# Kernel optimization log

Measured on AMD Instinct MI355X. Metric: run time of the kernel, lower is better.

## Reference

```python
import jax, jax.numpy as jnp
import numpy as np
import math

B, S, D, L, FF = 16, 2048, 512, 4, 2048
VOCAB, ATTR_VOCAB, MAXPOS = 33, 608, 2048
EPS = 1e-5


def layernorm(x, w, b):
    mu = jnp.mean(x, axis=-1, keepdims=True)
    var = jnp.mean(jnp.square(x - mu), axis=-1, keepdims=True)
    return (x - mu) * jax.lax.rsqrt(var + EPS) * w + b


def setup_inputs() -> dict:
    key = jax.random.key(0)
    ks = jax.random.split(key, 16)
    std = 0.02
    return {
        "input_ids": jax.random.randint(ks[0], (B, S), 0, VOCAB),
        "combined_indices": jax.random.randint(ks[1], (B,), 0, ATTR_VOCAB),
        "attention_mask": jnp.ones((B, S), dtype=jnp.float32),
        "tok_emb": jax.random.normal(ks[2], (VOCAB, D), jnp.float32) * std,
        "pos_emb": jax.random.normal(ks[3], (MAXPOS, D), jnp.float32) * std,
        "attr_emb": jax.random.normal(ks[4], (ATTR_VOCAB, D), jnp.float32) * std,
        "ln_w": jnp.ones((L, D), jnp.float32),
        "ln_b": jnp.zeros((L, D), jnp.float32),
        "w1": jax.random.normal(ks[5], (L, D, FF), jnp.float32) * std,
        "b1": jnp.zeros((L, FF), jnp.float32),
        "w2": jax.random.normal(ks[6], (L, FF, D), jnp.float32) * std,
        "b2": jnp.zeros((L, D), jnp.float32),
        "out_w": jax.random.normal(ks[7], (D, VOCAB), jnp.float32) * std,
        "out_b": jnp.zeros((VOCAB,), jnp.float32),
    }


def reference(input_ids, combined_indices, attention_mask, tok_emb, pos_emb,
              attr_emb, ln_w, ln_b, w1, b1, w2, b2, out_w, out_b):
    scale = 1.0 / math.sqrt(D)
    # embeddings: token + position + per-example attribute (broadcast over seq)
    x = tok_emb[input_ids] + pos_emb[jnp.arange(S)][None, :, :] \
        + attr_emb[combined_indices][:, None, :]
    mask_add = (1.0 - attention_mask)[:, None, :] * -1e9  # [B,1,S]
    for l in range(L):
        h = layernorm(x, ln_w[l], ln_b[l])                 # shared LN params used twice
        scores = jnp.einsum('bsd,btd->bst', h, h) * scale + mask_add
        probs = jax.nn.softmax(scores, axis=-1)            # dropout=0 (eval)
        attn = jnp.einsum('bst,btd->bsd', probs, h) + x    # residual
        n2 = layernorm(attn, ln_w[l], ln_b[l])
        ff = jax.nn.gelu(n2 @ w1[l] + b1[l], approximate=False) @ w2[l] + b2[l]
        x = ff + attn
    return x @ out_w + out_b
```

## Files before the change

### kernel.cpp

```cpp
#include <hip/hip_runtime.h>
#include <hip/hip_bf16.h>
#include <cmath>

#define B_ 16
#define S_ 2048
#define D_ 512
#define L_ 4
#define FF_ 2048
#define V_ 33

typedef unsigned short u16;
typedef __attribute__((ext_vector_type(8))) short bf16x8;
typedef __attribute__((ext_vector_type(4))) float f32x4;

__device__ __forceinline__ u16 f2bf(float f) {
    unsigned x = __float_as_uint(f);
    unsigned r = (x + 0x7fffu + ((x >> 16) & 1u)) >> 16;
    return (u16)r;
}
__device__ __forceinline__ float bf2f(u16 u) { return __uint_as_float(((unsigned)u) << 16); }

__device__ __forceinline__ float wave_sum(float v) {
#pragma unroll
    for (int o = 32; o; o >>= 1) v += __shfl_xor(v, o);
    return v;
}

__device__ __forceinline__ void gload16(const u16* g, u16* l) {
    __builtin_amdgcn_global_load_lds((const __attribute__((address_space(1))) void*)g,
                                     (__attribute__((address_space(3))) void*)l, 16, 0, 0);
}

__device__ __forceinline__ uint4 pack8(const u16* ov) {
    uint4 p;
    p.x = (unsigned)ov[0] | ((unsigned)ov[1] << 16);
    p.y = (unsigned)ov[2] | ((unsigned)ov[3] << 16);
    p.z = (unsigned)ov[4] | ((unsigned)ov[5] << 16);
    p.w = (unsigned)ov[6] | ((unsigned)ov[7] << 16);
    return p;
}

__global__ __launch_bounds__(256) void embed_kernel(
    const int* __restrict__ ids, const int* __restrict__ attr,
    const float* __restrict__ tok, const float* __restrict__ pos,
    const float* __restrict__ attre, float* __restrict__ x)
{
    int idx = blockIdx.x * 256 + threadIdx.x;
    const int total = B_ * S_ * (D_ / 4);
    if (idx >= total) return;
    int d4 = idx & (D_ / 4 - 1);
    int bs = idx >> 7;
    int s  = bs & (S_ - 1);
    int b  = bs >> 11;
    int id = ids[bs];
    int a  = attr[b];
    float4 t  = ((const float4*)tok)[id * (D_ / 4) + d4];
    float4 p  = ((const float4*)pos)[s * (D_ / 4) + d4];
    float4 at = ((const float4*)attre)[a * (D_ / 4) + d4];
    float4 o;
    o.x = t.x + p.x + at.x; o.y = t.y + p.y + at.y;
    o.z = t.z + p.z + at.z; o.w = t.w + p.w + at.w;
    ((float4*)x)[idx] = o;
}

__global__ __launch_bounds__(256) void ln_kernel(
    const float* __restrict__ in, u16* __restrict__ out,
    const float* __restrict__ w, const float* __restrict__ b, int rows)
{
    int gw = (int)((blockIdx.x * 256 + threadIdx.x) >> 6);
    int lane = threadIdx.x & 63;
    if (gw >= rows) return;
    const float4* p = (const float4*)(in + (size_t)gw * D_);
    float4 a0 = p[lane * 2], a1 = p[lane * 2 + 1];
    float xv[8] = {a0.x, a0.y, a0.z, a0.w, a1.x, a1.y, a1.z, a1.w};
    float s = 0.f;
#pragma unroll
    for (int k = 0; k < 8; k++) s += xv[k];
    s = wave_sum(s);
    float mu = s * (1.f / D_);
    float q = 0.f;
#pragma unroll
    for (int k = 0; k < 8; k++) { float d = xv[k] - mu; q += d * d; }
    q = wave_sum(q);
    float rs = rsqrtf(q * (1.f / D_) + 1e-5f);
    const float4* w4 = (const float4*)w;
    const float4* b4 = (const float4*)b;
    float4 w0 = w4[lane * 2], w1v = w4[lane * 2 + 1];
    float4 b0 = b4[lane * 2], b1v = b4[lane * 2 + 1];
    float wv[8] = {w0.x, w0.y, w0.z, w0.w, w1v.x, w1v.y, w1v.z, w1v.w};
    float bv[8] = {b0.x, b0.y, b0.z, b0.w, b1v.x, b1v.y, b1v.z, b1v.w};
    u16 ov[8];
#pragma unroll
    for (int k = 0; k < 8; k++) ov[k] = f2bf((xv[k] - mu) * rs * wv[k] + bv[k]);
    *(uint4*)(out + (size_t)gw * D_ + lane * 8) = pack8(ov);
}

__device__ __forceinline__ float toF(float v) { return v; }
__device__ __forceinline__ float toF(u16 v) { return bf2f(v); }

template <typename T>
__global__ void transpose_bf(const T* __restrict__ in, u16* __restrict__ out,
                             int R, int C, size_t sIn, size_t sOut)
{
    __shared__ float tile[32][33];
    const T* ip = in + (size_t)blockIdx.z * sIn;
    u16* op = out + (size_t)blockIdx.z * sOut;
    int tx = threadIdx.x, ty = threadIdx.y;
    int c = blockIdx.x * 32 + tx;
#pragma unroll
    for (int i = 0; i < 4; i++) {
        int r = blockIdx.y * 32 + ty + i * 8;
        tile[ty + i * 8][tx] = toF(ip[(size_t)r * C + c]);
    }
    __syncthreads();
#pragma unroll
    for (int i = 0; i < 4; i++) {
        int oc = blockIdx.x * 32 + ty + i * 8;
        op[(size_t)oc * R + blockIdx.y * 32 + tx] = f2bf(tile[tx][ty + i * 8]);
    }
}

__global__ __launch_bounds__(256) void rowsum_kernel(
    const u16* __restrict__ P, float* __restrict__ l, int rows)
{
    int gw = (int)((blockIdx.x * 256 + threadIdx.x) >> 6);
    int lane = threadIdx.x & 63;
    if (gw >= rows) return;
    const u16* pr = P + (size_t)gw * S_;
    float s = 0.f;
#pragma unroll
    for (int k = 0; k < 4; k++) {
        uint4 pk = *(const uint4*)(pr + k * 512 + lane * 8);
        s += bf2f((u16)(pk.x & 0xffff)) + bf2f((u16)(pk.x >> 16));
        s += bf2f((u16)(pk.y & 0xffff)) + bf2f((u16)(pk.y >> 16));
        s += bf2f((u16)(pk.z & 0xffff)) + bf2f((u16)(pk.z >> 16));
        s += bf2f((u16)(pk.w & 0xffff)) + bf2f((u16)(pk.w >> 16));
    }
    s = wave_sum(s);
    if (lane == 0) l[gw] = s;
}

enum { E_SC = 0, E_PV = 1, E_GELU = 2, E_FF2 = 3 };

template <int EPI>
__global__ __launch_bounds__(256) void gemm_nt(
    const u16* __restrict__ A, size_t sAz, int lda,
    const u16* __restrict__ B, size_t sBz, int ldb,
    float* Cf, u16* Cb, size_t sCz, int ldc,
    int K, float scale,
    const float* resid, size_t sRz,
    const float* __restrict__ bias,
    const float* __restrict__ aux, int b0)
{
    __shared__ __align__(16) u16 ldsA[128 * 64];
    __shared__ __align__(16) u16 ldsB[128 * 64];

    const int gx = gridDim.x, gy = gridDim.y;
    const int nwg = gx * gy * gridDim.z;
    int lid = blockIdx.x + gx * (blockIdx.y + gy * blockIdx.z);
    {
        const int q = nwg >> 3, r = nwg & 7;
        const int xcd = lid & 7, idx = lid >> 3;
        lid = (xcd < r ? xcd * (q + 1) : r * (q + 1) + (xcd - r) * q) + idx;
    }
    const int bx = lid % gx;
    const int t2 = lid / gx;
    const int by = t2 % gy;
    const int z  = t2 / gy;

    A += (size_t)z * sAz;
    B += (size_t)z * sBz;
    const size_t coff = (size_t)z * sCz;
    const int brow = by * 128, bcol = bx * 128;
    const int tid = threadIdx.x, lane = tid & 63, wid = tid >> 6;
    const int wr = wid >> 1, wc = wid & 1;

    f32x4 acc[4][4];
#pragma unroll
    for (int m = 0; m < 4; m++)
#pragma unroll
        for (int n = 0; n < 4; n++) acc[m][n] = 0.0f;

    const int lg   = lane >> 3;
    const int srow = wid * 8 + lg;
    const int skk  = ((lane & 7) ^ lg) << 3;

    const int l15 = lane & 15, l7 = lane & 7, kh = lane >> 4;

    for (int k0 = 0; k0 < K; k0 += 64) {
        __syncthreads();
#pragma unroll
        for (int r = 0; r < 4; r++) {
            const u16* ga = A + (size_t)(brow + r * 32 + srow) * lda + (k0 + skk);
            const u16* gb = B + (size_t)(bcol + r * 32 + srow) * ldb + (k0 + skk);
            gload16(ga, &ldsA[r * 2048 + wid * 512]);
            gload16(gb, &ldsB[r * 2048 + wid * 512]);
        }
        __syncthreads();
#pragma unroll
        for (int kk = 0; kk < 64; kk += 32) {
            const int kc = (kk >> 3) + kh;
            const int kswz = ((kc ^ l7) << 3);
            bf16x8 af[4], bfv[4];
#pragma unroll
            for (int m = 0; m < 4; m++)
                af[m] = *(const bf16x8*)&ldsA[(wr * 64 + m * 16 + l15) * 64 + kswz];
#pragma unroll
            for (int n = 0; n < 4; n++)
                bfv[n] = *(const bf16x8*)&ldsB[(wc * 64 + n * 16 + l15) * 64 + kswz];
#pragma unroll
            for (int m = 0; m < 4; m++)
#pragma unroll
                for (int n = 0; n < 4; n++)
                    acc[m][n] = __builtin_amdgcn_mfma_f32_16x16x32_bf16(af[m], bfv[n], acc[m][n], 0, 0, 0);
        }
    }

#pragma unroll
    for (int m = 0; m < 4; m++)
#pragma unroll
        for (int n = 0; n < 4; n++) {
            int rowb = brow + wr * 64 + m * 16 + ((lane >> 4) << 2);
            int col  = bcol + wc * 64 + n * 16 + l15;
#pragma unroll
            for (int j = 0; j < 4; j++) {
                int row = rowb + j;
                float v = acc[m][n][j];
                size_t off = coff + (size_t)row * ldc + col;
                if constexpr (EPI == E_SC) {
                    float mv = aux[(size_t)(b0 + z) * S_ + col];
                    Cb[off] = f2bf(__expf(v * scale + (1.f - mv) * -1e9f));
                } else if constexpr (EPI == E_PV) {
                    float lv = aux[(size_t)z * S_ + row];
                    Cf[off] = v / lv + resid[(size_t)z * sRz + (size_t)row * ldc + col];
                } else if constexpr (EPI == E_GELU) {
                    float t = v + bias[col];
                    Cb[off] = f2bf(0.5f * t * (1.f + erff(t * 0.70710678118f)));
                } else {
                    Cf[off] = v + bias[col] + resid[(size_t)row * ldc + col];
                }
            }
        }
}

#define WTS 72
__global__ __launch_bounds__(256) void outproj_kernel(
    const float* __restrict__ x, const float* __restrict__ W,
    const float* __restrict__ bias, float* __restrict__ out)
{
    __shared__ __align__(16) u16 WT[V_ * 8 * WTS];
    __shared__ float obuf[32][V_ + 1];
    for (int j = threadIdx.x; j < V_ * 8 * 64; j += 256) {
        int e = j & 63, t = j >> 6;
        int kc = t & 7, v = t >> 3;
        WT[(v * 8 + kc) * WTS + e] = f2bf(W[(kc * 64 + e) * V_ + v]);
    }
    __syncthreads();

    const int tid = threadIdx.x, lane = tid & 63, wid = tid >> 6;
    const int kc = lane >> 3;
    const int r  = lane & 7;
    const int row = blockIdx.x * 32 + wid * 8 + r;
    const float4* xr = (const float4*)(x + (size_t)row * D_) + kc * 16;

    float xv[64];
#pragma unroll
    for (int j = 0; j < 16; j++) {
        float4 t = xr[j];
        xv[j * 4 + 0] = t.x; xv[j * 4 + 1] = t.y;
        xv[j * 4 + 2] = t.z; xv[j * 4 + 3] = t.w;
    }

#pragma unroll
    for (int v = 0; v < V_; v++) {
        const bf16x8* wr = (const bf16x8*)&WT[(v * 8 + kc) * WTS];
        float p = 0.f;
#pragma unroll
        for (int j = 0; j < 8; j++) {
            bf16x8 wv = wr[j];
#pragma unroll
            for (int k = 0; k < 8; k++)
                p += xv[j * 8 + k] * bf2f((u16)wv[k]);
        }
        p += __shfl_xor(p, 8);
        p += __shfl_xor(p, 16);
        p += __shfl_xor(p, 32);
        if (kc == 0) obuf[wid * 8 + r][v] = p + bias[v];
    }
    __syncthreads();
    float* ob = out + (size_t)blockIdx.x * (32 * V_);
#pragma unroll 1
    for (int i = tid; i < 32 * V_; i += 256) {
        ob[i] = obuf[i / V_][i % V_];
    }
}

extern "C" void kernel_launch(void* const* d_in, const int* in_sizes, int n_in,
                              void* d_out, int out_size, void* d_ws, size_t ws_size,
                              hipStream_t stream)
{
    const int*   input_ids = (const int*)d_in[0];
    const int*   comb      = (const int*)d_in[1];
    const float* amask     = (const float*)d_in[2];
    const float* tok       = (const float*)d_in[3];
    const float* pos       = (const float*)d_in[4];
    const float* attre     = (const float*)d_in[5];
    const float* ln_w      = (const float*)d_in[6];
    const float* ln_b      = (const float*)d_in[7];
    const float* w1        = (const float*)d_in[8];
    const float* b1        = (const float*)d_in[9];
    const float* w2        = (const float*)d_in[10];
    const float* b2        = (const float*)d_in[11];
    const float* out_w     = (const float*)d_in[12];
    const float* out_b     = (const float*)d_in[13];
    float* out = (float*)d_out;
    (void)in_sizes; (void)n_in; (void)out_size;

    int NB_A, RC;
    if      (ws_size >= 281000000ULL) { NB_A = 16; RC = 32768; }
    else if (ws_size >= 176000000ULL) { NB_A = 8;  RC = 16384; }
    else if (ws_size >= 126000000ULL) { NB_A = 4;  RC = 8192;  }
    else                              { NB_A = 2;  RC = 4096;  }
    const int HR = NB_A * S_;

    unsigned char* ws = (unsigned char*)d_ws;
    size_t off = 0;
    auto carve = [&](size_t bytes) {
        void* p = ws + off;
        off += (bytes + 255) & ~(size_t)255;
        return p;
    };
    float* x    = (float*)carve((size_t)B_ * S_ * D_ * 4);
    u16* w1t    = (u16*)carve((size_t)D_ * FF_ * 2);
    u16* w2t    = (u16*)carve((size_t)D_ * FF_ * 2);
    u16* h      = (u16*)carve((size_t)HR * D_ * 2);
    u16* hT     = (u16*)carve((size_t)NB_A * S_ * D_ * 2);
    float* lsum = (float*)carve((size_t)NB_A * S_ * 4);
    size_t scP_bytes  = (size_t)NB_A * S_ * S_ * 2;
    size_t tbuf_bytes = (size_t)RC * FF_ * 2;
    void* un = carve(scP_bytes > tbuf_bytes ? scP_bytes : tbuf_bytes);
    u16* scP  = (u16*)un;
    u16* tbuf = (u16*)un;

    const float scl = 1.0f / sqrtf((float)D_);
    const int nG = B_ / NB_A;
    const int nC = (B_ * S_) / RC;

    embed_kernel<<<(B_ * S_ * (D_ / 4)) / 256, 256, 0, stream>>>(input_ids, comb, tok, pos, attre, x);

    for (int l = 0; l < L_; l++) {
        const float* lw = ln_w + l * D_;
        const float* lb = ln_b + l * D_;

        for (int g = 0; g < nG; g++) {
            float* xg = x + (size_t)g * NB_A * S_ * D_;
            ln_kernel<<<(NB_A * S_) / 4, 256, 0, stream>>>(xg, h, lw, lb, NB_A * S_);
            transpose_bf<u16><<<dim3(D_ / 32, S_ / 32, NB_A), dim3(32, 8), 0, stream>>>(
                h, hT, S_, D_, (size_t)S_ * D_, (size_t)S_ * D_);
            gemm_nt<E_SC><<<dim3(S_ / 128, S_ / 128, NB_A), 256, 0, stream>>>(
                h, (size_t)S_ * D_, D_,
                h, (size_t)S_ * D_, D_,
                nullptr, scP, (size_t)S_ * S_, S_,
                D_, scl, nullptr, 0, nullptr, amask, g * NB_A);
            rowsum_kernel<<<(NB_A * S_) / 4, 256, 0, stream>>>(scP, lsum, NB_A * S_);
            gemm_nt<E_PV><<<dim3(D_ / 128, S_ / 128, NB_A), 256, 0, stream>>>(
                scP, (size_t)S_ * S_, S_,
                hT, (size_t)S_ * D_, S_,
                xg, nullptr, (size_t)S_ * D_, D_,
                S_, 1.f, xg, (size_t)S_ * D_, nullptr, lsum, 0);
        }

        transpose_bf<float><<<dim3(FF_ / 32, D_ / 32, 1), dim3(32, 8), 0, stream>>>(
            w1 + (size_t)l * D_ * FF_, w1t, D_, FF_, 0, 0);
        transpose_bf<float><<<dim3(D_ / 32, FF_ / 32, 1), dim3(32, 8), 0, stream>>>(
            w2 + (size_t)l * FF_ * D_, w2t, FF_, D_, 0, 0);

        for (int c = 0; c < nC; c++) {
            size_t roff = (size_t)c * RC;
            ln_kernel<<<RC / 4, 256, 0, stream>>>(x + roff * D_, h, lw, lb, RC);
            gemm_nt<E_GELU><<<dim3(FF_ / 128, RC / 128, 1), 256, 0, stream>>>(
                h, 0, D_,
                w1t, 0, D_,
                nullptr, tbuf, 0, FF_,
                D_, 1.f, nullptr, 0, b1 + l * FF_, nullptr, 0);
            gemm_nt<E_FF2><<<dim3(D_ / 128, RC / 128, 1), 256, 0, stream>>>(
                tbuf, 0, FF_,
                w2t, 0, FF_,
                x + roff * D_, nullptr, 0, D_,
                FF_, 1.f, x + roff * D_, 0, b2 + l * D_, nullptr, 0);
        }
    }

    outproj_kernel<<<(B_ * S_) / 32, 256, 0, stream>>>(x, out_w, out_b, out);
}
```

Before: 2.179 ms.

## Fuse softmax row sums into score GEMM, hoist weight transposes, MFMA output projection

The score GEMM epilogue now accumulates per-row partial sums of the exponentiated scores and writes them to a small buffer, so the second full read of the bf16 probability matrix is replaced by a tiny reduction over 32 partials. The per-layer weight transposes are hoisted to a single batched launch before the layer loop, and the output projection is rewritten to use bf16 MFMA with a pre-transposed, padded weight. In exchange it uses more workspace, with raised thresholds for picking the batch-group size, and the MFMA output path rounds activations to bf16.

Result: faster. 2.115 ms (-2.9%).

```diff
diff --git a/kernel.cpp b/kernel.cpp
--- a/kernel.cpp
+++ b/kernel.cpp
@@ -120,24 +120,15 @@
     }
 }
 
-__global__ __launch_bounds__(256) void rowsum_kernel(
-    const u16* __restrict__ P, float* __restrict__ l, int rows)
-{
-    int gw = (int)((blockIdx.x * 256 + threadIdx.x) >> 6);
-    int lane = threadIdx.x & 63;
-    if (gw >= rows) return;
-    const u16* pr = P + (size_t)gw * S_;
+__global__ __launch_bounds__(256) void rowred_kernel(
+    const float* __restrict__ psum, float* __restrict__ lsum, int rows)
+{
+    int row = blockIdx.x * 256 + threadIdx.x;
+    if (row >= rows) return;
     float s = 0.f;
 #pragma unroll
-    for (int k = 0; k < 4; k++) {
-        uint4 pk = *(const uint4*)(pr + k * 512 + lane * 8);
-        s += bf2f((u16)(pk.x & 0xffff)) + bf2f((u16)(pk.x >> 16));
-        s += bf2f((u16)(pk.y & 0xffff)) + bf2f((u16)(pk.y >> 16));
-        s += bf2f((u16)(pk.z & 0xffff)) + bf2f((u16)(pk.z >> 16));
-        s += bf2f((u16)(pk.w & 0xffff)) + bf2f((u16)(pk.w >> 16));
-    }
-    s = wave_sum(s);
-    if (lane == 0) l[gw] = s;
+    for (int i = 0; i < 32; i++) s += psum[(size_t)i * rows + row];
+    lsum[row] = s;
 }
 
 enum { E_SC = 0, E_PV = 1, E_GELU = 2, E_FF2 = 3 };
@@ -150,7 +141,8 @@
     int K, float scale,
     const float* resid, size_t sRz,
     const float* __restrict__ bias,
-    const float* __restrict__ aux, int b0)
+    const float* __restrict__ aux, int b0,
+    float* __restrict__ psum)
 {
     __shared__ __align__(16) u16 ldsA[128 * 64];
     __shared__ __align__(16) u16 ldsB[128 * 64];
@@ -216,6 +208,12 @@
         }
     }
 
+    float rsum[4][4];
+#pragma unroll
+    for (int m = 0; m < 4; m++)
+#pragma unroll
+        for (int j = 0; j < 4; j++) rsum[m][j] = 0.f;
+
 #pragma unroll
     for (int m = 0; m < 4; m++)
 #pragma unroll
@@ -229,7 +227,9 @@
                 size_t off = coff + (size_t)row * ldc + col;
                 if constexpr (EPI == E_SC) {
                     float mv = aux[(size_t)(b0 + z) * S_ + col];
-                    Cb[off] = f2bf(__expf(v * scale + (1.f - mv) * -1e9f));
+                    float ev = __expf(v * scale + (1.f - mv) * -1e9f);
+                    Cb[off] = f2bf(ev);
+                    rsum[m][j] += ev;
                 } else if constexpr (EPI == E_PV) {
                     float lv = aux[(size_t)z * S_ + row];
                     Cf[off] = v / lv + resid[(size_t)z * sRz + (size_t)row * ldc + col];
@@ -241,58 +241,108 @@
                 }
             }
         }
-}
-
-#define WTS 72
-__global__ __launch_bounds__(256) void outproj_kernel(
-    const float* __restrict__ x, const float* __restrict__ W,
+
+    if constexpr (EPI == E_SC) {
+        const int nrows = gridDim.z * S_;
+#pragma unroll
+        for (int m = 0; m < 4; m++) {
+            int rowl = brow + wr * 64 + m * 16 + ((lane >> 4) << 2);
+#pragma unroll
+            for (int j = 0; j < 4; j++) {
+                float s = rsum[m][j];
+                s += __shfl_xor(s, 1);
+                s += __shfl_xor(s, 2);
+                s += __shfl_xor(s, 4);
+                s += __shfl_xor(s, 8);
+                if (l15 == 0)
+                    psum[(size_t)(bx * 2 + wc) * nrows + (size_t)z * S_ + rowl + j] = s;
+            }
+        }
+    }
+}
+
+__global__ __launch_bounds__(256) void wtb_kernel(
+    const float* __restrict__ W, u16* __restrict__ WTb)
+{
+    int i = blockIdx.x * 256 + threadIdx.x;
+    if (i >= 64 * 512) return;
+    int n = i >> 9, k = i & 511;
+    WTb[i] = f2bf(n < V_ ? W[k * V_ + n] : 0.f);
+}
+
+__global__ __launch_bounds__(256) void outproj_mfma(
+    const float* __restrict__ x, const u16* __restrict__ WTb,
     const float* __restrict__ bias, float* __restrict__ out)
 {
-    __shared__ __align__(16) u16 WT[V_ * 8 * WTS];
-    __shared__ float obuf[32][V_ + 1];
-    for (int j = threadIdx.x; j < V_ * 8 * 64; j += 256) {
-        int e = j & 63, t = j >> 6;
-        int kc = t & 7, v = t >> 3;
-        WT[(v * 8 + kc) * WTS + e] = f2bf(W[(kc * 64 + e) * V_ + v]);
-    }
+    __shared__ __align__(16) u16 ldsA[128 * 64];
+    __shared__ __align__(16) u16 ldsB[64 * 64];
+    __shared__ float obuf[128][34];
+    const int brow = blockIdx.x * 128;
+    const int tid = threadIdx.x, lane = tid & 63, wid = tid >> 6;
+    const int wr = wid >> 1, wc = wid & 1;
+    const int l15 = lane & 15, l7 = lane & 7, kh = lane >> 4;
+    const int lg = lane >> 3, srow = wid * 8 + lg;
+    const int skk = ((lane & 7) ^ lg) << 3;
+    const int ar = tid >> 1, ah = (tid & 1) * 32;
+
+    f32x4 acc[4][2];
+#pragma unroll
+    for (int m = 0; m < 4; m++)
+#pragma unroll
+        for (int n = 0; n < 2; n++) acc[m][n] = 0.0f;
+
+    for (int k0 = 0; k0 < 512; k0 += 64) {
+        __syncthreads();
+#pragma unroll
+        for (int r = 0; r < 2; r++)
+            gload16(WTb + (size_t)(r * 32 + srow) * 512 + (k0 + skk),
+                    &ldsB[r * 2048 + wid * 512]);
+        const float4* xs = (const float4*)(x + (size_t)(brow + ar) * 512 + k0 + ah);
+#pragma unroll
+        for (int j = 0; j < 4; j++) {
+            float4 a = xs[j * 2], b = xs[j * 2 + 1];
+            u16 t[8] = {f2bf(a.x), f2bf(a.y), f2bf(a.z), f2bf(a.w),
+                        f2bf(b.x), f2bf(b.y), f2bf(b.z), f2bf(b.w)};
+            int kc = (ah >> 3) + j;
+            *(uint4*)&ldsA[ar * 64 + ((kc ^ (ar & 7)) << 3)] = pack8(t);
+        }
+        __syncthreads();
+#pragma unroll
+        for (int kk = 0; kk < 64; kk += 32) {
+            const int kc = (kk >> 3) + kh;
+            const int kswz = ((kc ^ l7) << 3);
+            bf16x8 af[4], bfv[2];
+#pragma unroll
+            for (int m = 0; m < 4; m++)
+                af[m] = *(const bf16x8*)&ldsA[(wr * 64 + m * 16 + l15) * 64 + kswz];
+#pragma unroll
+            for (int n = 0; n < 2; n++)
+                bfv[n] = *(const bf16x8*)&ldsB[(wc * 32 + n * 16 + l15) * 64 + kswz];
+#pragma unroll
+            for (int m = 0; m < 4; m++)
+#pragma unroll
+                for (int n = 0; n < 2; n++)
+                    acc[m][n] = __builtin_amdgcn_mfma_f32_16x16x32_bf16(af[m], bfv[n], acc[m][n], 0, 0, 0);
+        }
+    }
+
+#pragma unroll
+    for (int m = 0; m < 4; m++)
+#pragma unroll
+        for (int n = 0; n < 2; n++) {
+            int rowl = wr * 64 + m * 16 + ((lane >> 4) << 2);
+            int col  = wc * 32 + n * 16 + l15;
+            if (col < V_) {
+#pragma unroll
+                for (int j = 0; j < 4; j++)
+                    obuf[rowl + j][col] = acc[m][n][j] + bias[col];
+            }
+        }
     __syncthreads();
-
-    const int tid = threadIdx.x, lane = tid & 63, wid = tid >> 6;
-    const int kc = lane >> 3;
-    const int r  = lane & 7;
-    const int row = blockIdx.x * 32 + wid * 8 + r;
-    const float4* xr = (const float4*)(x + (size_t)row * D_) + kc * 16;
-
-    float xv[64];
-#pragma unroll
-    for (int j = 0; j < 16; j++) {
-        float4 t = xr[j];
-        xv[j * 4 + 0] = t.x; xv[j * 4 + 1] = t.y;
-        xv[j * 4 + 2] = t.z; xv[j * 4 + 3] = t.w;
-    }
-
-#pragma unroll
-    for (int v = 0; v < V_; v++) {
-        const bf16x8* wr = (const bf16x8*)&WT[(v * 8 + kc) * WTS];
-        float p = 0.f;
-#pragma unroll
-        for (int j = 0; j < 8; j++) {
-            bf16x8 wv = wr[j];
-#pragma unroll
-            for (int k = 0; k < 8; k++)
-                p += xv[j * 8 + k] * bf2f((u16)wv[k]);
-        }
-        p += __shfl_xor(p, 8);
-        p += __shfl_xor(p, 16);
-        p += __shfl_xor(p, 32);
-        if (kc == 0) obuf[wid * 8 + r][v] = p + bias[v];
-    }
-    __syncthreads();
-    float* ob = out + (size_t)blockIdx.x * (32 * V_);
+    float* ob = out + (size_t)brow * V_;
 #pragma unroll 1
-    for (int i = tid; i < 32 * V_; i += 256) {
+    for (int i = tid; i < 128 * V_; i += 256)
         ob[i] = obuf[i / V_][i % V_];
-    }
 }
 
 extern "C" void kernel_launch(void* const* d_in, const int* in_sizes, int n_in,
@@ -317,9 +367,9 @@
     (void)in_sizes; (void)n_in; (void)out_size;
 
     int NB_A, RC;
-    if      (ws_size >= 281000000ULL) { NB_A = 16; RC = 32768; }
-    else if (ws_size >= 176000000ULL) { NB_A = 8;  RC = 16384; }
-    else if (ws_size >= 126000000ULL) { NB_A = 4;  RC = 8192;  }
+    if      (ws_size >= 335000000ULL) { NB_A = 16; RC = 32768; }
+    else if (ws_size >= 215000000ULL) { NB_A = 8;  RC = 16384; }
+    else if (ws_size >= 152000000ULL) { NB_A = 4;  RC = 8192;  }
     else                              { NB_A = 2;  RC = 4096;  }
     const int HR = NB_A * S_;
 
@@ -331,11 +381,13 @@
         return p;
     };
     float* x    = (float*)carve((size_t)B_ * S_ * D_ * 4);
-    u16* w1t    = (u16*)carve((size_t)D_ * FF_ * 2);
-    u16* w2t    = (u16*)carve((size_t)D_ * FF_ * 2);
+    u16* w1t    = (u16*)carve((size_t)L_ * D_ * FF_ * 2);
+    u16* w2t    = (u16*)carve((size_t)L_ * D_ * FF_ * 2);
     u16* h      = (u16*)carve((size_t)HR * D_ * 2);
     u16* hT     = (u16*)carve((size_t)NB_A * S_ * D_ * 2);
     float* lsum = (float*)carve((size_t)NB_A * S_ * 4);
+    float* psum = (float*)carve((size_t)NB_A * S_ * 32 * 4);
+    u16* WTb    = (u16*)carve((size_t)64 * 512 * 2);
     size_t scP_bytes  = (size_t)NB_A * S_ * S_ * 2;
     size_t tbuf_bytes = (size_t)RC * FF_ * 2;
     void* un = carve(scP_bytes > tbuf_bytes ? scP_bytes : tbuf_bytes);
@@ -347,6 +399,11 @@
     const int nC = (B_ * S_) / RC;
 
     embed_kernel<<<(B_ * S_ * (D_ / 4)) / 256, 256, 0, stream>>>(input_ids, comb, tok, pos, attre, x);
+    transpose_bf<float><<<dim3(FF_ / 32, D_ / 32, L_), dim3(32, 8), 0, stream>>>(
+        w1, w1t, D_, FF_, (size_t)D_ * FF_, (size_t)FF_ * D_);
+    transpose_bf<float><<<dim3(D_ / 32, FF_ / 32, L_), dim3(32, 8), 0, stream>>>(
+        w2, w2t, FF_, D_, (size_t)FF_ * D_, (size_t)D_ * FF_);
+    wtb_kernel<<<128, 256, 0, stream>>>(out_w, WTb);
 
     for (int l = 0; l < L_; l++) {
         const float* lw = ln_w + l * D_;
@@ -361,35 +418,30 @@
                 h, (size_t)S_ * D_, D_,
                 h, (size_t)S_ * D_, D_,
                 nullptr, scP, (size_t)S_ * S_, S_,
-                D_, scl, nullptr, 0, nullptr, amask, g * NB_A);
-            rowsum_kernel<<<(NB_A * S_) / 4, 256, 0, stream>>>(scP, lsum, NB_A * S_);
+                D_, scl, nullptr, 0, nullptr, amask, g * NB_A, psum);
+            rowred_kernel<<<(NB_A * S_ + 255) / 256, 256, 0, stream>>>(psum, lsum, NB_A * S_);
             gemm_nt<E_PV><<<dim3(D_ / 128, S_ / 128, NB_A), 256, 0, stream>>>(
                 scP, (size_t)S_ * S_, S_,
                 hT, (size_t)S_ * D_, S_,
                 xg, nullptr, (size_t)S_ * D_, D_,
-                S_, 1.f, xg, (size_t)S_ * D_, nullptr, lsum, 0);
-        }
-
-        transpose_bf<float><<<dim3(FF_ / 32, D_ / 32, 1), dim3(32, 8), 0, stream>>>(
-            w1 + (size_t)l * D_ * FF_, w1t, D_, FF_, 0, 0);
-        transpose_bf<float><<<dim3(D_ / 32, FF_ / 32, 1), dim3(32, 8), 0, stream>>>(
-            w2 + (size_t)l * FF_ * D_, w2t, FF_, D_, 0, 0);
+                S_, 1.f, xg, (size_t)S_ * D_, nullptr, lsum, 0, nullptr);
+        }
 
         for (int c = 0; c < nC; c++) {
             size_t roff = (size_t)c * RC;
             ln_kernel<<<RC / 4, 256, 0, stream>>>(x + roff * D_, h, lw, lb, RC);
             gemm_nt<E_GELU><<<dim3(FF_ / 128, RC / 128, 1), 256, 0, stream>>>(
                 h, 0, D_,
-                w1t, 0, D_,
+                w1t + (size_t)l * FF_ * D_, 0, D_,
                 nullptr, tbuf, 0, FF_,
-                D_, 1.f, nullptr, 0, b1 + l * FF_, nullptr, 0);
+                D_, 1.f, nullptr, 0, b1 + l * FF_, nullptr, 0, nullptr);
             gemm_nt<E_FF2><<<dim3(D_ / 128, RC / 128, 1), 256, 0, stream>>>(
                 tbuf, 0, FF_,
-                w2t, 0, FF_,
+                w2t + (size_t)l * D_ * FF_, 0, FF_,
                 x + roff * D_, nullptr, 0, D_,
-                FF_, 1.f, x + roff * D_, 0, b2 + l * D_, nullptr, 0);
-        }
-    }
-
-    outproj_kernel<<<(B_ * S_) / 32, 256, 0, stream>>>(x, out_w, out_b, out);
-}
+                FF_, 1.f, x + roff * D_, 0, b2 + l * D_, nullptr, 0, nullptr);
+        }
+    }
+
+    outproj_mfma<<<(B_ * S_) / 128, 256, 0, stream>>>(x, WTb, out_b, out);
+}
```
